# Kernel optimization log

Measured on AMD Instinct MI355X. Metric: run time of the kernel, lower is better.

## Reference

```python
import jax, jax.numpy as jnp
import numpy as np

N, NF, DIM, H, DH, DEPTH, EDIM, NB = 256, 127, 128, 8, 64, 6, 3, 512
INNER = H * DH  # 512
SCALE = DH ** -0.5
EPS = 1e-5


def setup_inputs() -> dict:
    key = jax.random.key(0)
    ks = jax.random.split(key, 16)
    p = lambda k, shape: jax.random.normal(k, shape, jnp.float32) * 0.02
    return {
        "coordinates": jax.random.normal(ks[0], (N, 3), jnp.float32),
        "bonds": jax.random.randint(ks[1], (NB, 2), 0, N),
        "noise_level": jax.random.uniform(ks[2], (1,), jnp.float32),
        "atom_emb": p(ks[3], (N, NF)),
        "ln1_g": jnp.ones((DEPTH, DIM)), "ln1_b": jnp.zeros((DEPTH, DIM)),
        "Wq": p(ks[4], (DEPTH, DIM, INNER)), "bq": jnp.zeros((DEPTH, INNER)),
        "Wkv": p(ks[5], (DEPTH, DIM, 2 * INNER)), "bkv": jnp.zeros((DEPTH, 2 * INNER)),
        "We": p(ks[6], (DEPTH, EDIM, INNER)), "be": jnp.zeros((DEPTH, INNER)),
        "Wo": p(ks[7], (DEPTH, INNER, DIM)), "bo": jnp.zeros((DEPTH, DIM)),
        "Wg1": p(ks[8], (DEPTH, 3 * DIM)),
        "ln2_g": jnp.ones((DEPTH, DIM)), "ln2_b": jnp.zeros((DEPTH, DIM)),
        "W1": p(ks[9], (DEPTH, DIM, 4 * DIM)), "b1": jnp.zeros((DEPTH, 4 * DIM)),
        "W2": p(ks[10], (DEPTH, 4 * DIM, DIM)), "b2": jnp.zeros((DEPTH, DIM)),
        "Wg2": p(ks[11], (DEPTH, 3 * DIM)),
        "out_w": p(ks[12], (DIM, 1)), "out_b": jnp.zeros((1,)),
    }


def _layernorm(x, g, b):
    m = jnp.mean(x, axis=-1, keepdims=True)
    v = jnp.mean((x - m) ** 2, axis=-1, keepdims=True)
    return (x - m) * jax.lax.rsqrt(v + EPS) * g + b


def _gated_residual(x, res, Wg):
    # Linear(3*dim -> 1, no bias) then sigmoid; mask is all-True so no masking.
    gate = jax.nn.sigmoid(jnp.concatenate([x, res, x - res], axis=-1) @ Wg)[..., None]
    return x * gate + res * (1.0 - gate)


def _forward(coordinates, bonds, noise_level, atom_emb, ln1_g, ln1_b, Wq, bq,
             Wkv, bkv, We, be, Wo, bo, Wg1, ln2_g, ln2_b, W1, b1, W2, b2, Wg2,
             out_w, out_b):
    n = coordinates.shape[0]
    # nodes: [n, NF] atom embeddings (looked up at arange(n)) + noise column -> [n, DIM]
    noise_col = jnp.broadcast_to(noise_level.reshape(1, 1), (n, 1))
    nodes = jnp.concatenate([atom_emb, noise_col], axis=-1)
    # dense edge tensor [n, n, 3]: coordinate differences at bonded pairs, antisymmetric
    bi, bj = bonds[:, 0], bonds[:, 1]
    diff = coordinates[bi] - coordinates[bj]
    edges = jnp.zeros((n, n, EDIM), jnp.float32).at[bi, bj].set(diff).at[bj, bi].set(-diff)

    for l in range(DEPTH):
        # --- edge-biased multi-head attention (PreNorm) ---
        x = _layernorm(nodes, ln1_g[l], ln1_b[l])
        q = (x @ Wq[l] + bq[l]).reshape(n, H, DH).transpose(1, 0, 2)          # [h, i, d]
        kv = x @ Wkv[l] + bkv[l]
        k = kv[:, :INNER].reshape(n, H, DH).transpose(1, 0, 2)                # [h, j, d]
        v = kv[:, INNER:].reshape(n, H, DH).transpose(1, 0, 2)                # [h, j, d]
        e = (edges @ We[l] + be[l]).reshape(n, n, H, DH).transpose(2, 0, 1, 3)  # [h, i, j, d]
        k_ij = k[:, None, :, :] + e                                            # [h, i, j, d]
        v_ij = v[:, None, :, :] + e
        sim = jnp.einsum('hid,hijd->hij', q, k_ij) * SCALE
        attn = jax.nn.softmax(sim, axis=-1)  # mask is all ones -> no-op
        out = jnp.einsum('hij,hijd->hid', attn, v_ij)                          # [h, i, d]
        out = out.transpose(1, 0, 2).reshape(n, INNER) @ Wo[l] + bo[l]         # [n, DIM]
        nodes = _gated_residual(out, nodes, Wg1[l])
        # --- feedforward (PreNorm) + gated residual ---
        y = _layernorm(nodes, ln2_g[l], ln2_b[l])
        y = jax.nn.gelu(y @ W1[l] + b1[l], approximate=False) @ W2[l] + b2[l]
        nodes = _gated_residual(y, nodes, Wg2[l])

    energy = nodes @ out_w + out_b  # [n, 1]
    return energy[None, :, :]       # [1, n, 1]


def reference(coordinates, bonds, noise_level, atom_emb, ln1_g, ln1_b, Wq, bq,
              Wkv, bkv, We, be, Wo, bo, Wg1, ln2_g, ln2_b, W1, b1, W2, b2, Wg2,
              out_w, out_b):
    return _forward(coordinates, bonds, noise_level, atom_emb, ln1_g, ln1_b,
                    Wq, bq, Wkv, bkv, We, be, Wo, bo, Wg1, ln2_g, ln2_b,
                    W1, b1, W2, b2, Wg2, out_w, out_b)
```

## Files before the change

kernel.cpp:

```cpp
#include <hip/hip_runtime.h>

#define NN     256
#define NF     127
#define DIM    128
#define NH     8
#define DH     64
#define INNER  512
#define DEPTH  6
#define NB     512
#define ATTN_SCALE 0.125f
#define LN_EPS 1e-5f

#define FMA4(A_, S_, V_) { A_.x=fmaf(S_,(V_).x,A_.x); A_.y=fmaf(S_,(V_).y,A_.y); \
                           A_.z=fmaf(S_,(V_).z,A_.z); A_.w=fmaf(S_,(V_).w,A_.w); }

__device__ __forceinline__ float wred_sum(float v){
#pragma unroll
  for(int o=32;o;o>>=1) v += __shfl_xor(v,o);
  return v;
}
__device__ __forceinline__ float wred_max(float v){
#pragma unroll
  for(int o=32;o;o>>=1) v = fmaxf(v,__shfl_xor(v,o));
  return v;
}
__device__ __forceinline__ float2 wred_sum2(float a, float b){
#pragma unroll
  for(int o=32;o;o>>=1){ a += __shfl_xor(a,o); b += __shfl_xor(b,o); }
  return make_float2(a,b);
}

__device__ __forceinline__ void ln_wave(float n0, float n1,
                                        const float* g, const float* b, int l,
                                        float& x0, float& x1){
  float2 sv = wred_sum2(n0+n1, n0*n0+n1*n1);
  float m  = sv.x*(1.f/DIM);
  float var = sv.y*(1.f/DIM) - m*m;
  float rs = rsqrtf(var + LN_EPS);
  x0 = (n0-m)*rs*g[l]    + b[l];
  x1 = (n1-m)*rs*g[64+l] + b[64+l];
}

__device__ __forceinline__ void gate_wave(float o0, float o1, float& n0, float& n1,
                                          const float* Wg, int l){
  float gv = o0*Wg[l]    + n0*Wg[DIM+l]    + (o0-n0)*Wg[2*DIM+l]
           + o1*Wg[64+l] + n1*Wg[DIM+64+l] + (o1-n1)*Wg[2*DIM+64+l];
  gv = wred_sum(gv);
  float gate = 1.f/(1.f + expf(-gv));
  n0 = o0*gate + n0*(1.f-gate);
  n1 = o1*gate + n1*(1.f-gate);
}

__device__ __forceinline__ void mvp128_512(const float* xin, const float* W,
                                           float* SC, int t){
  const int cg4 = (t&127)<<2, fq = t>>7;
  float4 acc = make_float4(0.f,0.f,0.f,0.f);
#pragma unroll 8
  for(int f=fq*32; f<fq*32+32; f++){
    float4 wv = *(const float4*)(W + f*INNER + cg4);
    float xv = xin[f];
    FMA4(acc, xv, wv);
  }
  *(float4*)(SC + fq*INNER + cg4) = acc;
}
__device__ __forceinline__ void mvp128_1024(const float* xin, const float* W,
                                            float* SC, int t){
  const int cg4 = (t&255)<<2, rh = t>>8;
  float4 acc = make_float4(0.f,0.f,0.f,0.f);
#pragma unroll 8
  for(int f=rh*64; f<rh*64+64; f++){
    float4 wv = *(const float4*)(W + f*(2*INNER) + cg4);
    float xv = xin[f];
    FMA4(acc, xv, wv);
  }
  *(float4*)(SC + rh*(2*INNER) + cg4) = acc;
}
__device__ __forceinline__ void mvp512_128(const float* ain, const float* W,
                                           float* SC, int t){
  const int cg4 = (t&31)<<2, fg = t>>5;
  float4 acc = make_float4(0.f,0.f,0.f,0.f);
#pragma unroll 8
  for(int f=fg*32; f<fg*32+32; f++){
    float4 wv = *(const float4*)(W + f*DIM + cg4);
    float av = ain[f];
    FMA4(acc, av, wv);
  }
  *(float4*)(SC + fg*DIM + cg4) = acc;
}

__device__ __forceinline__ void qkv_tail(const float* xs, int i,
    const float* Wq, const float* bq, const float* Wkv, const float* bkv,
    const float* be, float* qgn, float* kTn, float* vgn, float* SC, int t){
  mvp128_512(xs, Wq, SC, t);
  __syncthreads();
  qgn[i*INNER + t] = bq[t] + SC[t] + SC[INNER+t] + SC[2*INNER+t] + SC[3*INNER+t];
  __syncthreads();
  mvp128_1024(xs, Wkv, SC, t);
  __syncthreads();
#pragma unroll
  for(int cc=0; cc<2; cc++){
    int c = t + cc*512;
    float s = bkv[c] + SC[c] + SC[2*INNER+c];
    if(c < INNER) kTn[c*NN + i]            = s + be[c];
    else          vgn[i*INNER + c - INNER] = s + be[c-INNER];
  }
}

__global__ __launch_bounds__(512) void k_qkv0(const float* atom_emb, const float* noise,
    float* nodes, const float* ln1_g, const float* ln1_b,
    const float* Wq, const float* bq, const float* Wkv, const float* bkv, const float* be,
    float* qg, float* kT, float* vg){
  __shared__ __align__(16) float SC[2048];
  __shared__ __align__(16) float xsm[DIM];
  const int t = threadIdx.x, i = blockIdx.x;
  const int w = t>>6, l = t&63;
  float nd0 = (l<NF)?    atom_emb[i*NF + l]      : noise[0];
  float nd1 = (64+l<NF)? atom_emb[i*NF + 64 + l] : noise[0];
  if(w==0){ nodes[i*DIM + l] = nd0; nodes[i*DIM + 64 + l] = nd1; }
  float x0, x1;
  ln_wave(nd0, nd1, ln1_g, ln1_b, l, x0, x1);
  xsm[l] = x0; xsm[64+l] = x1;
  __syncthreads();
  qkv_tail(xsm, i, Wq, bq, Wkv, bkv, be, qg, kT, vg, SC, t);
}

__global__ __launch_bounds__(512) void k_attn(
    const float* qg, const float* kT, const float* vg,
    const int* bonds, const float* coords, const float* We,
    float* aog)
{
  __shared__ __align__(16) float qsm[8*DH];
  __shared__ __align__(16) float eb[8][3*NN];
  __shared__ __align__(16) float aW[8][NN];
  const int t = threadIdx.x;
  const int h = blockIdx.x >> 5, i0 = (blockIdx.x & 31) << 3;
  const int w = t>>6, l = t&63;
  const int qb = h*DH, j0 = l<<2;

  qsm[w*DH + l] = qg[(i0+w)*INNER + qb + l];
#pragma unroll
  for(int cc=0; cc<12; cc++) (&eb[0][0])[cc*512 + t] = 0.f;
  __syncthreads();

  {
    const int bi = bonds[2*t], bj = bonds[2*t+1];
    const bool hi = (bi>=i0 && bi<i0+8), hj = (bj>=i0 && bj<i0+8);
    if(hi || hj){
      float dx = coords[3*bi+0] - coords[3*bj+0];
      float dy = coords[3*bi+1] - coords[3*bj+1];
      float dz = coords[3*bi+2] - coords[3*bj+2];
      if(hi){ float* e = eb[bi-i0]; e[bj]=dx;  e[NN+bj]=dy;  e[2*NN+bj]=dz;  }
      if(hj){ float* e = eb[bj-i0]; e[bi]=-dx; e[NN+bi]=-dy; e[2*NN+bi]=-dz; }
    }
  }
  __syncthreads();

  float qwe0, qwe1, qwe2;
  {
    float qv = qsm[w*DH + l];
    qwe0 = qv*We[0*INNER + qb + l];
    qwe1 = qv*We[1*INNER + qb + l];
    qwe2 = qv*We[2*INNER + qb + l];
#pragma unroll
    for(int o=32;o;o>>=1){
      qwe0 += __shfl_xor(qwe0,o); qwe1 += __shfl_xor(qwe1,o); qwe2 += __shfl_xor(qwe2,o);
    }
  }
  const float* kTh = kT + qb*NN;
  float s0=0.f,s1=0.f,s2=0.f,s3=0.f;
#pragma unroll 8
  for(int o=0;o<DH;o++){
    float qv = qsm[w*DH + o];
    float4 kk = *(const float4*)(kTh + o*NN + j0);
    s0=fmaf(qv,kk.x,s0); s1=fmaf(qv,kk.y,s1); s2=fmaf(qv,kk.z,s2); s3=fmaf(qv,kk.w,s3);
  }
  const float* e = eb[w];
  float4 ex = *(const float4*)(e + j0);
  float4 ey = *(const float4*)(e + NN + j0);
  float4 ez = *(const float4*)(e + 2*NN + j0);
  s0 = (s0 + qwe0*ex.x + qwe1*ey.x + qwe2*ez.x)*ATTN_SCALE;
  s1 = (s1 + qwe0*ex.y + qwe1*ey.y + qwe2*ez.y)*ATTN_SCALE;
  s2 = (s2 + qwe0*ex.z + qwe1*ey.z + qwe2*ez.z)*ATTN_SCALE;
  s3 = (s3 + qwe0*ex.w + qwe1*ey.w + qwe2*ez.w)*ATTN_SCALE;
  float mx = wred_max(fmaxf(fmaxf(s0,s1),fmaxf(s2,s3)));
  float p0=expf(s0-mx), p1=expf(s1-mx), p2=expf(s2-mx), p3=expf(s3-mx);
  float inv = 1.f / wred_sum(p0+p1+p2+p3);
  float a0=p0*inv, a1=p1*inv, a2=p2*inv, a3=p3*inv;
  *(float4*)(aW[w] + j0) = make_float4(a0,a1,a2,a3);
  float c0 = a0*ex.x + a1*ex.y + a2*ex.z + a3*ex.w;
  float c1 = a0*ey.x + a1*ey.y + a2*ey.z + a3*ey.w;
  float c2 = a0*ez.x + a1*ez.y + a2*ez.z + a3*ez.w;
  c0 = wred_sum(c0); c1 = wred_sum(c1); c2 = wred_sum(c2);
  __builtin_amdgcn_wave_barrier();
  const int dq = (l&15)<<2, jg = l>>4;
  const float* vb = vg + qb + dq;
  float4 acc = make_float4(0.f,0.f,0.f,0.f);
#pragma unroll 8
  for(int jj=0;jj<64;jj++){
    int j = (jg<<6) + ((jj + (jg<<3)) & 63);
    float a = aW[w][j];
    float4 vv = *(const float4*)(vb + j*INNER);
    FMA4(acc, a, vv);
  }
#pragma unroll
  for(int o=16;o<64;o<<=1){
    acc.x += __shfl_xor(acc.x,o); acc.y += __shfl_xor(acc.y,o);
    acc.z += __shfl_xor(acc.z,o); acc.w += __shfl_xor(acc.w,o);
  }
  if(l<16){
    float4 we0 = *(const float4*)(We + 0*INNER + qb + dq);
    float4 we1 = *(const float4*)(We + 1*INNER + qb + dq);
    float4 we2 = *(const float4*)(We + 2*INNER + qb + dq);
    float4 ov;
    ov.x = acc.x + c0*we0.x + c1*we1.x + c2*we2.x;
    ov.y = acc.y + c0*we0.y + c1*we1.y + c2*we2.y;
    ov.z = acc.z + c0*we0.z + c1*we1.z + c2*we2.z;
    ov.w = acc.w + c0*we0.w + c1*we1.w + c2*we2.w;
    *(float4*)(aog + (i0+w)*INNER + qb + dq) = ov;
  }
}

__global__ __launch_bounds__(512) void k_layer(
    float* nodes, const float* aog,
    float* qg_n, float* kT_n, float* vg_n,
    const float* Wo, const float* bo, const float* Wg1,
    const float* ln2_g, const float* ln2_b,
    const float* W1, const float* b1, const float* W2, const float* b2,
    const float* Wg2,
    const float* ln1_g_n, const float* ln1_b_n,
    const float* Wq_n, const float* bq_n, const float* Wkv_n, const float* bkv_n,
    const float* be_n,
    const float* out_w, const float* out_b, float* eout, int has_next)
{
  __shared__ __align__(16) float SC[2048];
  __shared__ __align__(16) float qs[INNER];
  __shared__ __align__(16) float aos[INNER];
  __shared__ __align__(16) float xsm[DIM];
  const int t = threadIdx.x, i = blockIdx.x;
  const int w = t>>6, l = t&63;

  aos[t] = aog[i*INNER + t];
  float nd0 = nodes[i*DIM + l];
  float nd1 = nodes[i*DIM + 64 + l];
  __syncthreads();

  mvp512_128(aos, Wo, SC, t);
  __syncthreads();
  {
    float o0 = bo[l], o1 = bo[64+l];
#pragma unroll
    for(int fg=0; fg<16; fg++){ o0 += SC[fg*DIM + l]; o1 += SC[fg*DIM + 64 + l]; }
    gate_wave(o0, o1, nd0, nd1, Wg1, l);
    float x0, x1;
    ln_wave(nd0, nd1, ln2_g, ln2_b, l, x0, x1);
    xsm[l] = x0; xsm[64+l] = x1;
  }
  __syncthreads();

  mvp128_512(xsm, W1, SC, t);
  __syncthreads();
  {
    float a = b1[t] + SC[t] + SC[INNER+t] + SC[2*INNER+t] + SC[3*INNER+t];
    qs[t] = 0.5f*a*(1.f + erff(a*0.70710678118654752440f));
  }
  __syncthreads();
  mvp512_128(qs, W2, SC, t);
  __syncthreads();
  {
    float y0 = b2[l], y1 = b2[64+l];
#pragma unroll
    for(int fg=0; fg<16; fg++){ y0 += SC[fg*DIM + l]; y1 += SC[fg*DIM + 64 + l]; }
    gate_wave(y0, y1, nd0, nd1, Wg2, l);
    if(w==0){ nodes[i*DIM + l] = nd0; nodes[i*DIM + 64 + l] = nd1; }
    if(has_next){
      float x0, x1;
      ln_wave(nd0, nd1, ln1_g_n, ln1_b_n, l, x0, x1);
      xsm[l] = x0; xsm[64+l] = x1;
    } else if(w==0){
      float ev = nd0*out_w[l] + nd1*out_w[64+l];
      ev = wred_sum(ev);
      if(l==0) eout[i] = ev + out_b[0];
    }
  }
  if(has_next){
    __syncthreads();
    qkv_tail(xsm, i, Wq_n, bq_n, Wkv_n, bkv_n, be_n,
             qg_n, kT_n, vg_n, SC, t);
  }
}

extern "C" void kernel_launch(void* const* d_in, const int* in_sizes, int n_in,
                              void* d_out, int out_size, void* d_ws, size_t ws_size,
                              hipStream_t stream){
  const float* coords   = (const float*)d_in[0];
  const int*   bonds    = (const int*  )d_in[1];
  const float* noise    = (const float*)d_in[2];
  const float* atom_emb = (const float*)d_in[3];
  const float* ln1_g = (const float*)d_in[4];
  const float* ln1_b = (const float*)d_in[5];
  const float* Wq    = (const float*)d_in[6];
  const float* bq    = (const float*)d_in[7];
  const float* Wkv   = (const float*)d_in[8];
  const float* bkv   = (const float*)d_in[9];
  const float* We    = (const float*)d_in[10];
  const float* be    = (const float*)d_in[11];
  const float* Wo    = (const float*)d_in[12];
  const float* bo    = (const float*)d_in[13];
  const float* Wg1   = (const float*)d_in[14];
  const float* ln2_g = (const float*)d_in[15];
  const float* ln2_b = (const float*)d_in[16];
  const float* W1    = (const float*)d_in[17];
  const float* b1    = (const float*)d_in[18];
  const float* W2    = (const float*)d_in[19];
  const float* b2    = (const float*)d_in[20];
  const float* Wg2   = (const float*)d_in[21];
  const float* out_w = (const float*)d_in[22];
  const float* out_b = (const float*)d_in[23];

  float* ws = (float*)d_ws;
  float* nodes   = ws;
  float* qbuf[2] = { ws +  32768, ws + 163840 };
  float* kbuf[2] = { ws + 294912, ws + 425984 };
  float* vbuf[2] = { ws + 557056, ws + 688128 };
  float* aobuf   = ws + 819200;

  k_qkv0<<<NN, 512, 0, stream>>>(atom_emb, noise, nodes, ln1_g, ln1_b,
                                 Wq, bq, Wkv, bkv, be,
                                 qbuf[0], kbuf[0], vbuf[0]);
  for(int l=0; l<DEPTH; l++){
    int cur = l&1, nxt = cur^1;
    int has_next = (l < DEPTH-1);
    int ln = has_next ? l+1 : l;
    k_attn<<<NN, 512, 0, stream>>>(
      qbuf[cur], kbuf[cur], vbuf[cur], bonds, coords,
      We + (size_t)l*3*INNER, aobuf);
    k_layer<<<NN, 512, 0, stream>>>(
      nodes, aobuf,
      qbuf[nxt], kbuf[nxt], vbuf[nxt],
      Wo  + (size_t)l*INNER*DIM, bo + (size_t)l*DIM, Wg1 + (size_t)l*3*DIM,
      ln2_g + (size_t)l*DIM, ln2_b + (size_t)l*DIM,
      W1  + (size_t)l*DIM*4*DIM, b1 + (size_t)l*4*DIM,
      W2  + (size_t)l*4*DIM*DIM, b2 + (size_t)l*DIM, Wg2 + (size_t)l*3*DIM,
      ln1_g + (size_t)ln*DIM, ln1_b + (size_t)ln*DIM,
      Wq  + (size_t)ln*DIM*INNER, bq + (size_t)ln*INNER,
      Wkv + (size_t)ln*DIM*2*INNER, bkv + (size_t)ln*2*INNER,
      be  + (size_t)ln*INNER,
      out_w, out_b, (float*)d_out, has_next);
  }
}
```

Baseline: 303.6 us.

## Fuse all layers into one cooperative persistent kernel with grid syncs

```diff
diff --git a/kernel.cpp b/kernel.cpp
--- a/kernel.cpp
+++ b/kernel.cpp
@@ -1,4 +1,6 @@
 #include <hip/hip_runtime.h>
+#include <hip/hip_cooperative_groups.h>
+namespace cg = cooperative_groups;
 
 #define NN     256
 #define NF     127
@@ -106,186 +108,196 @@
   }
 }
 
-__global__ __launch_bounds__(512) void k_qkv0(const float* atom_emb, const float* noise,
-    float* nodes, const float* ln1_g, const float* ln1_b,
-    const float* Wq, const float* bq, const float* Wkv, const float* bkv, const float* be,
-    float* qg, float* kT, float* vg){
+__global__ __launch_bounds__(512) void k_net(
+    const float* coords, const int* bonds, const float* noise, const float* atom_emb,
+    const float* ln1_g, const float* ln1_b,
+    const float* Wq, const float* bq, const float* Wkv, const float* bkv,
+    const float* We, const float* be,
+    const float* Wo, const float* bo, const float* Wg1,
+    const float* ln2_g, const float* ln2_b,
+    const float* W1, const float* b1, const float* W2, const float* b2,
+    const float* Wg2, const float* out_w, const float* out_b,
+    float* q0, float* k0, float* v0, float* q1, float* k1, float* v1,
+    float* aog, float* eout)
+{
+  cg::grid_group grid = cg::this_grid();
   __shared__ __align__(16) float SC[2048];
+  __shared__ __align__(16) float qs[INNER];
+  __shared__ __align__(16) float aos[INNER];
   __shared__ __align__(16) float xsm[DIM];
-  const int t = threadIdx.x, i = blockIdx.x;
+  __shared__ __align__(16) float qsm[8*DH];
+  __shared__ __align__(16) float aW[8][NN];
+  __shared__ __align__(16) float eb[8][3*NN];
+
+  const int t = threadIdx.x, bid = blockIdx.x;
   const int w = t>>6, l = t&63;
+  const int i = bid;
+  const int ah = bid>>5, ai0 = (bid&31)<<3;
+  const int qb = ah*DH, j0 = l<<2;
+
   float nd0 = (l<NF)?    atom_emb[i*NF + l]      : noise[0];
   float nd1 = (64+l<NF)? atom_emb[i*NF + 64 + l] : noise[0];
-  if(w==0){ nodes[i*DIM + l] = nd0; nodes[i*DIM + 64 + l] = nd1; }
-  float x0, x1;
-  ln_wave(nd0, nd1, ln1_g, ln1_b, l, x0, x1);
-  xsm[l] = x0; xsm[64+l] = x1;
-  __syncthreads();
-  qkv_tail(xsm, i, Wq, bq, Wkv, bkv, be, qg, kT, vg, SC, t);
-}
-
-__global__ __launch_bounds__(512) void k_attn(
-    const float* qg, const float* kT, const float* vg,
-    const int* bonds, const float* coords, const float* We,
-    float* aog)
-{
-  __shared__ __align__(16) float qsm[8*DH];
-  __shared__ __align__(16) float eb[8][3*NN];
-  __shared__ __align__(16) float aW[8][NN];
-  const int t = threadIdx.x;
-  const int h = blockIdx.x >> 5, i0 = (blockIdx.x & 31) << 3;
-  const int w = t>>6, l = t&63;
-  const int qb = h*DH, j0 = l<<2;
-
-  qsm[w*DH + l] = qg[(i0+w)*INNER + qb + l];
+  {
+    float x0, x1;
+    ln_wave(nd0, nd1, ln1_g, ln1_b, l, x0, x1);
+    xsm[l] = x0; xsm[64+l] = x1;
+  }
 #pragma unroll
   for(int cc=0; cc<12; cc++) (&eb[0][0])[cc*512 + t] = 0.f;
   __syncthreads();
-
   {
     const int bi = bonds[2*t], bj = bonds[2*t+1];
-    const bool hi = (bi>=i0 && bi<i0+8), hj = (bj>=i0 && bj<i0+8);
+    const bool hi = (bi>=ai0 && bi<ai0+8), hj = (bj>=ai0 && bj<ai0+8);
     if(hi || hj){
       float dx = coords[3*bi+0] - coords[3*bj+0];
       float dy = coords[3*bi+1] - coords[3*bj+1];
       float dz = coords[3*bi+2] - coords[3*bj+2];
-      if(hi){ float* e = eb[bi-i0]; e[bj]=dx;  e[NN+bj]=dy;  e[2*NN+bj]=dz;  }
-      if(hj){ float* e = eb[bj-i0]; e[bi]=-dx; e[NN+bi]=-dy; e[2*NN+bi]=-dz; }
+      if(hi){ float* e = eb[bi-ai0]; e[bj]=dx;  e[NN+bj]=dy;  e[2*NN+bj]=dz;  }
+      if(hj){ float* e = eb[bj-ai0]; e[bi]=-dx; e[NN+bi]=-dy; e[2*NN+bi]=-dz; }
     }
   }
   __syncthreads();
-
-  float qwe0, qwe1, qwe2;
-  {
-    float qv = qsm[w*DH + l];
-    qwe0 = qv*We[0*INNER + qb + l];
-    qwe1 = qv*We[1*INNER + qb + l];
-    qwe2 = qv*We[2*INNER + qb + l];
-#pragma unroll
-    for(int o=32;o;o>>=1){
-      qwe0 += __shfl_xor(qwe0,o); qwe1 += __shfl_xor(qwe1,o); qwe2 += __shfl_xor(qwe2,o);
+  qkv_tail(xsm, i, Wq, bq, Wkv, bkv, be, q0, k0, v0, SC, t);
+  grid.sync();
+
+  for(int ly=0; ly<DEPTH; ly++){
+    const float* qcur = (ly&1)? q1:q0;
+    const float* kcur = (ly&1)? k1:k0;
+    const float* vcur = (ly&1)? v1:v0;
+    float* qnxt = (ly&1)? q0:q1;
+    float* knxt = (ly&1)? k0:k1;
+    float* vnxt = (ly&1)? v0:v1;
+    const float* Wel = We + (size_t)ly*3*INNER;
+
+    {
+      qsm[w*DH + l] = qcur[(ai0+w)*INNER + qb + l];
+      __syncthreads();
+      float qwe0, qwe1, qwe2;
+      {
+        float qv = qsm[w*DH + l];
+        qwe0 = qv*Wel[0*INNER + qb + l];
+        qwe1 = qv*Wel[1*INNER + qb + l];
+        qwe2 = qv*Wel[2*INNER + qb + l];
+#pragma unroll
+        for(int o=32;o;o>>=1){
+          qwe0 += __shfl_xor(qwe0,o); qwe1 += __shfl_xor(qwe1,o); qwe2 += __shfl_xor(qwe2,o);
+        }
+      }
+      const float* kTh = kcur + qb*NN;
+      float s0=0.f,s1=0.f,s2=0.f,s3=0.f;
+#pragma unroll 8
+      for(int o=0;o<DH;o++){
+        float qv = qsm[w*DH + o];
+        float4 kk = *(const float4*)(kTh + o*NN + j0);
+        s0=fmaf(qv,kk.x,s0); s1=fmaf(qv,kk.y,s1); s2=fmaf(qv,kk.z,s2); s3=fmaf(qv,kk.w,s3);
+      }
+      const float* e = eb[w];
+      float4 ex = *(const float4*)(e + j0);
+      float4 ey = *(const float4*)(e + NN + j0);
+      float4 ez = *(const float4*)(e + 2*NN + j0);
+      s0 = (s0 + qwe0*ex.x + qwe1*ey.x + qwe2*ez.x)*ATTN_SCALE;
+      s1 = (s1 + qwe0*ex.y + qwe1*ey.y + qwe2*ez.y)*ATTN_SCALE;
+      s2 = (s2 + qwe0*ex.z + qwe1*ey.z + qwe2*ez.z)*ATTN_SCALE;
+      s3 = (s3 + qwe0*ex.w + qwe1*ey.w + qwe2*ez.w)*ATTN_SCALE;
+      float mx = wred_max(fmaxf(fmaxf(s0,s1),fmaxf(s2,s3)));
+      float p0=expf(s0-mx), p1=expf(s1-mx), p2=expf(s2-mx), p3=expf(s3-mx);
+      float inv = 1.f / wred_sum(p0+p1+p2+p3);
+      float a0=p0*inv, a1=p1*inv, a2=p2*inv, a3=p3*inv;
+      *(float4*)(aW[w] + j0) = make_float4(a0,a1,a2,a3);
+      float c0 = a0*ex.x + a1*ex.y + a2*ex.z + a3*ex.w;
+      float c1 = a0*ey.x + a1*ey.y + a2*ey.z + a3*ey.w;
+      float c2 = a0*ez.x + a1*ez.y + a2*ez.z + a3*ez.w;
+      c0 = wred_sum(c0); c1 = wred_sum(c1); c2 = wred_sum(c2);
+      __builtin_amdgcn_wave_barrier();
+      const int dq = (l&15)<<2, jg = l>>4;
+      const float* vb = vcur + qb + dq;
+      float4 acc = make_float4(0.f,0.f,0.f,0.f);
+#pragma unroll 8
+      for(int jj=0;jj<64;jj++){
+        int j = (jg<<6) + ((jj + (jg<<3)) & 63);
+        float a = aW[w][j];
+        float4 vv = *(const float4*)(vb + j*INNER);
+        FMA4(acc, a, vv);
+      }
+#pragma unroll
+      for(int o=16;o<64;o<<=1){
+        acc.x += __shfl_xor(acc.x,o); acc.y += __shfl_xor(acc.y,o);
+        acc.z += __shfl_xor(acc.z,o); acc.w += __shfl_xor(acc.w,o);
+      }
+      if(l<16){
+        float4 we0 = *(const float4*)(Wel + 0*INNER + qb + dq);
+        float4 we1 = *(const float4*)(Wel + 1*INNER + qb + dq);
+        float4 we2 = *(const float4*)(Wel + 2*INNER + qb + dq);
+        float4 ov;
+        ov.x = acc.x + c0*we0.x + c1*we1.x + c2*we2.x;
+        ov.y = acc.y + c0*we0.y + c1*we1.y + c2*we2.y;
+        ov.z = acc.z + c0*we0.z + c1*we1.z + c2*we2.z;
+        ov.w = acc.w + c0*we0.w + c1*we1.w + c2*we2.w;
+        *(float4*)(aog + (ai0+w)*INNER + qb + dq) = ov;
+      }
     }
-  }
-  const float* kTh = kT + qb*NN;
-  float s0=0.f,s1=0.f,s2=0.f,s3=0.f;
-#pragma unroll 8
-  for(int o=0;o<DH;o++){
-    float qv = qsm[w*DH + o];
-    float4 kk = *(const float4*)(kTh + o*NN + j0);
-    s0=fmaf(qv,kk.x,s0); s1=fmaf(qv,kk.y,s1); s2=fmaf(qv,kk.z,s2); s3=fmaf(qv,kk.w,s3);
-  }
-  const float* e = eb[w];
-  float4 ex = *(const float4*)(e + j0);
-  float4 ey = *(const float4*)(e + NN + j0);
-  float4 ez = *(const float4*)(e + 2*NN + j0);
-  s0 = (s0 + qwe0*ex.x + qwe1*ey.x + qwe2*ez.x)*ATTN_SCALE;
-  s1 = (s1 + qwe0*ex.y + qwe1*ey.y + qwe2*ez.y)*ATTN_SCALE;
-  s2 = (s2 + qwe0*ex.z + qwe1*ey.z + qwe2*ez.z)*ATTN_SCALE;
-  s3 = (s3 + qwe0*ex.w + qwe1*ey.w + qwe2*ez.w)*ATTN_SCALE;
-  float mx = wred_max(fmaxf(fmaxf(s0,s1),fmaxf(s2,s3)));
-  float p0=expf(s0-mx), p1=expf(s1-mx), p2=expf(s2-mx), p3=expf(s3-mx);
-  float inv = 1.f / wred_sum(p0+p1+p2+p3);
-  float a0=p0*inv, a1=p1*inv, a2=p2*inv, a3=p3*inv;
-  *(float4*)(aW[w] + j0) = make_float4(a0,a1,a2,a3);
-  float c0 = a0*ex.x + a1*ex.y + a2*ex.z + a3*ex.w;
-  float c1 = a0*ey.x + a1*ey.y + a2*ey.z + a3*ey.w;
-  float c2 = a0*ez.x + a1*ez.y + a2*ez.z + a3*ez.w;
-  c0 = wred_sum(c0); c1 = wred_sum(c1); c2 = wred_sum(c2);
-  __builtin_amdgcn_wave_barrier();
-  const int dq = (l&15)<<2, jg = l>>4;
-  const float* vb = vg + qb + dq;
-  float4 acc = make_float4(0.f,0.f,0.f,0.f);
-#pragma unroll 8
-  for(int jj=0;jj<64;jj++){
-    int j = (jg<<6) + ((jj + (jg<<3)) & 63);
-    float a = aW[w][j];
-    float4 vv = *(const float4*)(vb + j*INNER);
-    FMA4(acc, a, vv);
-  }
-#pragma unroll
-  for(int o=16;o<64;o<<=1){
-    acc.x += __shfl_xor(acc.x,o); acc.y += __shfl_xor(acc.y,o);
-    acc.z += __shfl_xor(acc.z,o); acc.w += __shfl_xor(acc.w,o);
-  }
-  if(l<16){
-    float4 we0 = *(const float4*)(We + 0*INNER + qb + dq);
-    float4 we1 = *(const float4*)(We + 1*INNER + qb + dq);
-    float4 we2 = *(const float4*)(We + 2*INNER + qb + dq);
-    float4 ov;
-    ov.x = acc.x + c0*we0.x + c1*we1.x + c2*we2.x;
-    ov.y = acc.y + c0*we0.y + c1*we1.y + c2*we2.y;
-    ov.z = acc.z + c0*we0.z + c1*we1.z + c2*we2.z;
-    ov.w = acc.w + c0*we0.w + c1*we1.w + c2*we2.w;
-    *(float4*)(aog + (i0+w)*INNER + qb + dq) = ov;
-  }
-}
-
-__global__ __launch_bounds__(512) void k_layer(
-    float* nodes, const float* aog,
-    float* qg_n, float* kT_n, float* vg_n,
-    const float* Wo, const float* bo, const float* Wg1,
-    const float* ln2_g, const float* ln2_b,
-    const float* W1, const float* b1, const float* W2, const float* b2,
-    const float* Wg2,
-    const float* ln1_g_n, const float* ln1_b_n,
-    const float* Wq_n, const float* bq_n, const float* Wkv_n, const float* bkv_n,
-    const float* be_n,
-    const float* out_w, const float* out_b, float* eout, int has_next)
-{
-  __shared__ __align__(16) float SC[2048];
-  __shared__ __align__(16) float qs[INNER];
-  __shared__ __align__(16) float aos[INNER];
-  __shared__ __align__(16) float xsm[DIM];
-  const int t = threadIdx.x, i = blockIdx.x;
-  const int w = t>>6, l = t&63;
-
-  aos[t] = aog[i*INNER + t];
-  float nd0 = nodes[i*DIM + l];
-  float nd1 = nodes[i*DIM + 64 + l];
-  __syncthreads();
-
-  mvp512_128(aos, Wo, SC, t);
-  __syncthreads();
-  {
-    float o0 = bo[l], o1 = bo[64+l];
-#pragma unroll
-    for(int fg=0; fg<16; fg++){ o0 += SC[fg*DIM + l]; o1 += SC[fg*DIM + 64 + l]; }
-    gate_wave(o0, o1, nd0, nd1, Wg1, l);
-    float x0, x1;
-    ln_wave(nd0, nd1, ln2_g, ln2_b, l, x0, x1);
-    xsm[l] = x0; xsm[64+l] = x1;
-  }
-  __syncthreads();
-
-  mvp128_512(xsm, W1, SC, t);
-  __syncthreads();
-  {
-    float a = b1[t] + SC[t] + SC[INNER+t] + SC[2*INNER+t] + SC[3*INNER+t];
-    qs[t] = 0.5f*a*(1.f + erff(a*0.70710678118654752440f));
-  }
-  __syncthreads();
-  mvp512_128(qs, W2, SC, t);
-  __syncthreads();
-  {
-    float y0 = b2[l], y1 = b2[64+l];
-#pragma unroll
-    for(int fg=0; fg<16; fg++){ y0 += SC[fg*DIM + l]; y1 += SC[fg*DIM + 64 + l]; }
-    gate_wave(y0, y1, nd0, nd1, Wg2, l);
-    if(w==0){ nodes[i*DIM + l] = nd0; nodes[i*DIM + 64 + l] = nd1; }
-    if(has_next){
-      float x0, x1;
-      ln_wave(nd0, nd1, ln1_g_n, ln1_b_n, l, x0, x1);
-      xsm[l] = x0; xsm[64+l] = x1;
-    } else if(w==0){
-      float ev = nd0*out_w[l] + nd1*out_w[64+l];
-      ev = wred_sum(ev);
-      if(l==0) eout[i] = ev + out_b[0];
+    grid.sync();
+
+    {
+      const float* Wol = Wo + (size_t)ly*INNER*DIM;
+      const float* bol = bo + (size_t)ly*DIM;
+      const float* Wg1l = Wg1 + (size_t)ly*3*DIM;
+      const float* ln2gl = ln2_g + (size_t)ly*DIM;
+      const float* ln2bl = ln2_b + (size_t)ly*DIM;
+      const float* W1l = W1 + (size_t)ly*DIM*4*DIM;
+      const float* b1l = b1 + (size_t)ly*4*DIM;
+      const float* W2l = W2 + (size_t)ly*4*DIM*DIM;
+      const float* b2l = b2 + (size_t)ly*DIM;
+      const float* Wg2l = Wg2 + (size_t)ly*3*DIM;
+
+      aos[t] = aog[i*INNER + t];
+      __syncthreads();
+      mvp512_128(aos, Wol, SC, t);
+      __syncthreads();
+      {
+        float o0 = bol[l], o1 = bol[64+l];
+#pragma unroll
+        for(int fg=0; fg<16; fg++){ o0 += SC[fg*DIM + l]; o1 += SC[fg*DIM + 64 + l]; }
+        gate_wave(o0, o1, nd0, nd1, Wg1l, l);
+        float x0, x1;
+        ln_wave(nd0, nd1, ln2gl, ln2bl, l, x0, x1);
+        xsm[l] = x0; xsm[64+l] = x1;
+      }
+      __syncthreads();
+      mvp128_512(xsm, W1l, SC, t);
+      __syncthreads();
+      {
+        float a = b1l[t] + SC[t] + SC[INNER+t] + SC[2*INNER+t] + SC[3*INNER+t];
+        qs[t] = 0.5f*a*(1.f + erff(a*0.70710678118654752440f));
+      }
+      __syncthreads();
+      mvp512_128(qs, W2l, SC, t);
+      __syncthreads();
+      {
+        float y0 = b2l[l], y1 = b2l[64+l];
+#pragma unroll
+        for(int fg=0; fg<16; fg++){ y0 += SC[fg*DIM + l]; y1 += SC[fg*DIM + 64 + l]; }
+        gate_wave(y0, y1, nd0, nd1, Wg2l, l);
+        if(ly < DEPTH-1){
+          float x0, x1;
+          ln_wave(nd0, nd1, ln1_g + (size_t)(ly+1)*DIM, ln1_b + (size_t)(ly+1)*DIM, l, x0, x1);
+          xsm[l] = x0; xsm[64+l] = x1;
+        } else if(w==0){
+          float ev = nd0*out_w[l] + nd1*out_w[64+l];
+          ev = wred_sum(ev);
+          if(l==0) eout[i] = ev + out_b[0];
+        }
+      }
+      if(ly < DEPTH-1){
+        __syncthreads();
+        qkv_tail(xsm, i,
+                 Wq  + (size_t)(ly+1)*DIM*INNER,   bq  + (size_t)(ly+1)*INNER,
+                 Wkv + (size_t)(ly+1)*DIM*2*INNER, bkv + (size_t)(ly+1)*2*INNER,
+                 be  + (size_t)(ly+1)*INNER,
+                 qnxt, knxt, vnxt, SC, t);
+      }
     }
-  }
-  if(has_next){
-    __syncthreads();
-    qkv_tail(xsm, i, Wq_n, bq_n, Wkv_n, bkv_n, be_n,
-             qg_n, kT_n, vg_n, SC, t);
+    if(ly < DEPTH-1) grid.sync();
   }
 }
 
@@ -318,33 +330,27 @@
   const float* out_b = (const float*)d_in[23];
 
   float* ws = (float*)d_ws;
-  float* nodes   = ws;
-  float* qbuf[2] = { ws +  32768, ws + 163840 };
-  float* kbuf[2] = { ws + 294912, ws + 425984 };
-  float* vbuf[2] = { ws + 557056, ws + 688128 };
-  float* aobuf   = ws + 819200;
-
-  k_qkv0<<<NN, 512, 0, stream>>>(atom_emb, noise, nodes, ln1_g, ln1_b,
-                                 Wq, bq, Wkv, bkv, be,
-                                 qbuf[0], kbuf[0], vbuf[0]);
-  for(int l=0; l<DEPTH; l++){
-    int cur = l&1, nxt = cur^1;
-    int has_next = (l < DEPTH-1);
-    int ln = has_next ? l+1 : l;
-    k_attn<<<NN, 512, 0, stream>>>(
-      qbuf[cur], kbuf[cur], vbuf[cur], bonds, coords,
-      We + (size_t)l*3*INNER, aobuf);
-    k_layer<<<NN, 512, 0, stream>>>(
-      nodes, aobuf,
-      qbuf[nxt], kbuf[nxt], vbuf[nxt],
-      Wo  + (size_t)l*INNER*DIM, bo + (size_t)l*DIM, Wg1 + (size_t)l*3*DIM,
-      ln2_g + (size_t)l*DIM, ln2_b + (size_t)l*DIM,
-      W1  + (size_t)l*DIM*4*DIM, b1 + (size_t)l*4*DIM,
-      W2  + (size_t)l*4*DIM*DIM, b2 + (size_t)l*DIM, Wg2 + (size_t)l*3*DIM,
-      ln1_g + (size_t)ln*DIM, ln1_b + (size_t)ln*DIM,
-      Wq  + (size_t)ln*DIM*INNER, bq + (size_t)ln*INNER,
-      Wkv + (size_t)ln*DIM*2*INNER, bkv + (size_t)ln*2*INNER,
-      be  + (size_t)ln*INNER,
-      out_w, out_b, (float*)d_out, has_next);
-  }
-}
+  float* q0 = ws;
+  float* k0 = ws + 131072;
+  float* v0 = ws + 262144;
+  float* q1 = ws + 393216;
+  float* k1 = ws + 524288;
+  float* v1 = ws + 655360;
+  float* aog = ws + 786432;
+  float* eout = (float*)d_out;
+
+  void* args[] = {
+    (void*)&coords, (void*)&bonds, (void*)&noise, (void*)&atom_emb,
+    (void*)&ln1_g, (void*)&ln1_b,
+    (void*)&Wq, (void*)&bq, (void*)&Wkv, (void*)&bkv,
+    (void*)&We, (void*)&be,
+    (void*)&Wo, (void*)&bo, (void*)&Wg1,
+    (void*)&ln2_g, (void*)&ln2_b,
+    (void*)&W1, (void*)&b1, (void*)&W2, (void*)&b2,
+    (void*)&Wg2, (void*)&out_w, (void*)&out_b,
+    (void*)&q0, (void*)&k0, (void*)&v0, (void*)&q1, (void*)&k1, (void*)&v1,
+    (void*)&aog, (void*)&eout
+  };
+  hipLaunchCooperativeKernel((const void*)k_net, dim3(NN), dim3(512),
+                             (void**)args, 0, stream);
+}
```

Result: slower. 797.9 us (+162.8%).

## Precompute edge tensor once and prefetch next-layer weights into L2 during attention

Applied to the files above, without the earlier changes.

```diff
diff --git a/kernel.cpp b/kernel.cpp
--- a/kernel.cpp
+++ b/kernel.cpp
@@ -109,11 +109,34 @@
 __global__ __launch_bounds__(512) void k_qkv0(const float* atom_emb, const float* noise,
     float* nodes, const float* ln1_g, const float* ln1_b,
     const float* Wq, const float* bq, const float* Wkv, const float* bkv, const float* be,
-    float* qg, float* kT, float* vg){
+    float* qg, float* kT, float* vg,
+    const int* bonds, const float* coords, float* ebg){
   __shared__ __align__(16) float SC[2048];
   __shared__ __align__(16) float xsm[DIM];
-  const int t = threadIdx.x, i = blockIdx.x;
-  const int w = t>>6, l = t&63;
+  __shared__ __align__(16) float ebs[8*768];
+  const int t = threadIdx.x, bid = blockIdx.x;
+  if(bid >= NN){
+    const int i0 = (bid-NN)<<3;
+#pragma unroll
+    for(int cc=0; cc<12; cc++) ebs[cc*512 + t] = 0.f;
+    __syncthreads();
+    {
+      const int bi = bonds[2*t], bj = bonds[2*t+1];
+      const bool hi = (bi>=i0 && bi<i0+8), hj = (bj>=i0 && bj<i0+8);
+      if(hi || hj){
+        float dx = coords[3*bi+0] - coords[3*bj+0];
+        float dy = coords[3*bi+1] - coords[3*bj+1];
+        float dz = coords[3*bi+2] - coords[3*bj+2];
+        if(hi){ float* e = ebs + (bi-i0)*768; e[bj]=dx;  e[256+bj]=dy;  e[512+bj]=dz;  }
+        if(hj){ float* e = ebs + (bj-i0)*768; e[bi]=-dx; e[256+bi]=-dy; e[512+bi]=-dz; }
+      }
+    }
+    __syncthreads();
+#pragma unroll
+    for(int cc=0; cc<12; cc++) ebg[(size_t)i0*768 + cc*512 + t] = ebs[cc*512 + t];
+    return;
+  }
+  const int i = bid, w = t>>6, l = t&63;
   float nd0 = (l<NF)?    atom_emb[i*NF + l]      : noise[0];
   float nd1 = (64+l<NF)? atom_emb[i*NF + 64 + l] : noise[0];
   if(w==0){ nodes[i*DIM + l] = nd0; nodes[i*DIM + 64 + l] = nd1; }
@@ -125,12 +148,14 @@
 }
 
 __global__ __launch_bounds__(512) void k_attn(
-    const float* qg, const float* kT, const float* vg,
-    const int* bonds, const float* coords, const float* We,
-    float* aog)
+    const float* __restrict__ qg, const float* __restrict__ kT,
+    const float* __restrict__ vg, const float* __restrict__ ebg,
+    const float* __restrict__ We, float* __restrict__ aog,
+    const float* __restrict__ pfA, const float* __restrict__ pfB,
+    const float* __restrict__ pfC, const float* __restrict__ pfD,
+    const float* __restrict__ pfE, int pf_next)
 {
   __shared__ __align__(16) float qsm[8*DH];
-  __shared__ __align__(16) float eb[8][3*NN];
   __shared__ __align__(16) float aW[8][NN];
   const int t = threadIdx.x;
   const int h = blockIdx.x >> 5, i0 = (blockIdx.x & 31) << 3;
@@ -138,20 +163,19 @@
   const int qb = h*DH, j0 = l<<2;
 
   qsm[w*DH + l] = qg[(i0+w)*INNER + qb + l];
-#pragma unroll
-  for(int cc=0; cc<12; cc++) (&eb[0][0])[cc*512 + t] = 0.f;
-  __syncthreads();
-
-  {
-    const int bi = bonds[2*t], bj = bonds[2*t+1];
-    const bool hi = (bi>=i0 && bi<i0+8), hj = (bj>=i0 && bj<i0+8);
-    if(hi || hj){
-      float dx = coords[3*bi+0] - coords[3*bj+0];
-      float dy = coords[3*bi+1] - coords[3*bj+1];
-      float dz = coords[3*bi+2] - coords[3*bj+2];
-      if(hi){ float* e = eb[bi-i0]; e[bj]=dx;  e[NN+bj]=dy;  e[2*NN+bj]=dz;  }
-      if(hj){ float* e = eb[bj-i0]; e[bi]=-dx; e[NN+bi]=-dy; e[2*NN+bi]=-dz; }
+
+  {
+    const int s = blockIdx.x >> 3;
+    float keep = 0.f;
+    { float4 v = ((const float4*)pfA)[s*512 + t];  keep += v.x+v.y+v.z+v.w; }
+    { float4 v = ((const float4*)pfB)[s*512 + t];  keep += v.x+v.y+v.z+v.w; }
+    { float4 v = ((const float4*)pfC)[s*512 + t];  keep += v.x+v.y+v.z+v.w; }
+    if(pf_next){
+      { float4 v = ((const float4*)pfD)[s*512 + t];        keep += v.x+v.y+v.z+v.w; }
+      { float4 v = ((const float4*)pfE)[s*1024 + t];       keep += v.x+v.y+v.z+v.w; }
+      { float4 v = ((const float4*)pfE)[s*1024 + 512 + t]; keep += v.x+v.y+v.z+v.w; }
     }
+    asm volatile("" :: "v"(keep));
   }
   __syncthreads();
 
@@ -166,7 +190,7 @@
       qwe0 += __shfl_xor(qwe0,o); qwe1 += __shfl_xor(qwe1,o); qwe2 += __shfl_xor(qwe2,o);
     }
   }
-  const float* kTh = kT + qb*NN;
+  const float* __restrict__ kTh = kT + qb*NN;
   float s0=0.f,s1=0.f,s2=0.f,s3=0.f;
 #pragma unroll 8
   for(int o=0;o<DH;o++){
@@ -174,10 +198,10 @@
     float4 kk = *(const float4*)(kTh + o*NN + j0);
     s0=fmaf(qv,kk.x,s0); s1=fmaf(qv,kk.y,s1); s2=fmaf(qv,kk.z,s2); s3=fmaf(qv,kk.w,s3);
   }
-  const float* e = eb[w];
+  const float* __restrict__ e = ebg + (size_t)(i0+w)*768;
   float4 ex = *(const float4*)(e + j0);
-  float4 ey = *(const float4*)(e + NN + j0);
-  float4 ez = *(const float4*)(e + 2*NN + j0);
+  float4 ey = *(const float4*)(e + 256 + j0);
+  float4 ez = *(const float4*)(e + 512 + j0);
   s0 = (s0 + qwe0*ex.x + qwe1*ey.x + qwe2*ez.x)*ATTN_SCALE;
   s1 = (s1 + qwe0*ex.y + qwe1*ey.y + qwe2*ez.y)*ATTN_SCALE;
   s2 = (s2 + qwe0*ex.z + qwe1*ey.z + qwe2*ez.z)*ATTN_SCALE;
@@ -193,7 +217,7 @@
   c0 = wred_sum(c0); c1 = wred_sum(c1); c2 = wred_sum(c2);
   __builtin_amdgcn_wave_barrier();
   const int dq = (l&15)<<2, jg = l>>4;
-  const float* vb = vg + qb + dq;
+  const float* __restrict__ vb = vg + qb + dq;
   float4 acc = make_float4(0.f,0.f,0.f,0.f);
 #pragma unroll 8
   for(int jj=0;jj<64;jj++){
@@ -221,16 +245,20 @@
 }
 
 __global__ __launch_bounds__(512) void k_layer(
-    float* nodes, const float* aog,
+    float* nodes, const float* __restrict__ aog,
     float* qg_n, float* kT_n, float* vg_n,
-    const float* Wo, const float* bo, const float* Wg1,
-    const float* ln2_g, const float* ln2_b,
-    const float* W1, const float* b1, const float* W2, const float* b2,
-    const float* Wg2,
-    const float* ln1_g_n, const float* ln1_b_n,
-    const float* Wq_n, const float* bq_n, const float* Wkv_n, const float* bkv_n,
-    const float* be_n,
-    const float* out_w, const float* out_b, float* eout, int has_next)
+    const float* __restrict__ Wo, const float* __restrict__ bo,
+    const float* __restrict__ Wg1,
+    const float* __restrict__ ln2_g, const float* __restrict__ ln2_b,
+    const float* __restrict__ W1, const float* __restrict__ b1,
+    const float* __restrict__ W2, const float* __restrict__ b2,
+    const float* __restrict__ Wg2,
+    const float* __restrict__ ln1_g_n, const float* __restrict__ ln1_b_n,
+    const float* __restrict__ Wq_n, const float* __restrict__ bq_n,
+    const float* __restrict__ Wkv_n, const float* __restrict__ bkv_n,
+    const float* __restrict__ be_n,
+    const float* __restrict__ out_w, const float* __restrict__ out_b,
+    float* eout, int has_next)
 {
   __shared__ __align__(16) float SC[2048];
   __shared__ __align__(16) float qs[INNER];
@@ -323,27 +351,35 @@
   float* kbuf[2] = { ws + 294912, ws + 425984 };
   float* vbuf[2] = { ws + 557056, ws + 688128 };
   float* aobuf   = ws + 819200;
-
-  k_qkv0<<<NN, 512, 0, stream>>>(atom_emb, noise, nodes, ln1_g, ln1_b,
-                                 Wq, bq, Wkv, bkv, be,
-                                 qbuf[0], kbuf[0], vbuf[0]);
+  float* ebg     = ws + 950272;
+
+  k_qkv0<<<NN+32, 512, 0, stream>>>(atom_emb, noise, nodes, ln1_g, ln1_b,
+                                    Wq, bq, Wkv, bkv, be,
+                                    qbuf[0], kbuf[0], vbuf[0],
+                                    bonds, coords, ebg);
   for(int l=0; l<DEPTH; l++){
     int cur = l&1, nxt = cur^1;
     int has_next = (l < DEPTH-1);
     int ln = has_next ? l+1 : l;
+    const float* Wo_l = Wo + (size_t)l*INNER*DIM;
+    const float* W1_l = W1 + (size_t)l*DIM*4*DIM;
+    const float* W2_l = W2 + (size_t)l*4*DIM*DIM;
+    const float* Wq_n = Wq  + (size_t)ln*DIM*INNER;
+    const float* Wkv_n= Wkv + (size_t)ln*DIM*2*INNER;
     k_attn<<<NN, 512, 0, stream>>>(
-      qbuf[cur], kbuf[cur], vbuf[cur], bonds, coords,
-      We + (size_t)l*3*INNER, aobuf);
+      qbuf[cur], kbuf[cur], vbuf[cur], ebg,
+      We + (size_t)l*3*INNER, aobuf,
+      Wo_l, W1_l, W2_l, Wq_n, Wkv_n, has_next);
     k_layer<<<NN, 512, 0, stream>>>(
       nodes, aobuf,
       qbuf[nxt], kbuf[nxt], vbuf[nxt],
-      Wo  + (size_t)l*INNER*DIM, bo + (size_t)l*DIM, Wg1 + (size_t)l*3*DIM,
+      Wo_l, bo + (size_t)l*DIM, Wg1 + (size_t)l*3*DIM,
       ln2_g + (size_t)l*DIM, ln2_b + (size_t)l*DIM,
-      W1  + (size_t)l*DIM*4*DIM, b1 + (size_t)l*4*DIM,
-      W2  + (size_t)l*4*DIM*DIM, b2 + (size_t)l*DIM, Wg2 + (size_t)l*3*DIM,
+      W1_l, b1 + (size_t)l*4*DIM,
+      W2_l, b2 + (size_t)l*DIM, Wg2 + (size_t)l*3*DIM,
       ln1_g + (size_t)ln*DIM, ln1_b + (size_t)ln*DIM,
-      Wq  + (size_t)ln*DIM*INNER, bq + (size_t)ln*INNER,
-      Wkv + (size_t)ln*DIM*2*INNER, bkv + (size_t)ln*2*INNER,
+      Wq_n, bq + (size_t)ln*INNER,
+      Wkv_n, bkv + (size_t)ln*2*INNER,
       be  + (size_t)ln*INNER,
       out_w, out_b, (float*)d_out, has_next);
   }
```

After: 296.3 us. 1.02x faster.
